# Optimization experiments

Measured on AMD Instinct MI355X. Metric: run time of the kernel, lower is better.

The kernel has to match this reference:

```python
import jax, jax.numpy as jnp
import numpy as np

B, NPTS, T, P, C, D = 2, 32768, 32768, 512, 4, 768


def _sincos_pos_embed(centers, embed_dim):
    # centers: np [P,3]; matches get_3d_sincos_pos_embed
    c = centers - centers.mean(axis=0)
    c = c / np.linalg.norm(c, axis=1).max()
    div = np.exp(np.arange(0, embed_dim, 6) * -(np.log(10000.0) / embed_dim))  # [D/6]
    arg = c[:, None, :] * div[None, :, None]                                   # [P, D/6, 3]
    pe = np.concatenate([np.sin(arg), np.cos(arg)], axis=-1).reshape(centers.shape[0], embed_dim)
    return pe.astype(np.float32)


def setup_inputs() -> dict:
    key = jax.random.key(0)
    ks = jax.random.split(key, 12)
    rng = np.random.default_rng(0)

    # ragged patch sizes (avg 64) summing exactly to T
    sizes = rng.integers(32, 97, size=P).astype(np.int64)
    sizes = np.maximum((sizes * (T / sizes.sum())).astype(np.int64), 1)
    sizes[-1] += T - sizes.sum()
    patch_offset = jnp.asarray(np.concatenate([[0], np.cumsum(sizes)]), dtype=jnp.int32)  # [P+1]

    patch_index = jax.random.randint(ks[0], (T,), 0, NPTS, dtype=jnp.int32)
    latent = jax.random.normal(ks[1], (B, NPTS, C), dtype=jnp.float32)

    s = 0.02
    params = dict(
        w1a=jax.random.normal(ks[2], (C, D), jnp.float32) * s,
        b1a=jnp.zeros((D,), jnp.float32),
        w1b=jax.random.normal(ks[3], (D, D), jnp.float32) * s,
        b1b=jnp.zeros((D,), jnp.float32),
        w2a=jax.random.normal(ks[4], (2 * D, D), jnp.float32) * s,
        b2a=jnp.zeros((D,), jnp.float32),
        g2=jnp.ones((D,), jnp.float32),
        beta2=jnp.zeros((D,), jnp.float32),
        w2b=jax.random.normal(ks[5], (D, D), jnp.float32) * s,
        b2b=jnp.zeros((D,), jnp.float32),
    )

    centers = rng.standard_normal((P, 3))
    pos_embed = jnp.asarray(_sincos_pos_embed(centers, D))[None]  # [1, P, D]

    return dict(latent=latent, patch_index=patch_index, patch_offset=patch_offset,
                pos_embed=pos_embed, **params)


def _ln(x, eps, gamma=None, beta=None):
    mu = x.mean(axis=-1, keepdims=True)
    var = ((x - mu) ** 2).mean(axis=-1, keepdims=True)
    y = (x - mu) * jax.lax.rsqrt(var + eps)
    if gamma is not None:
        y = y * gamma + beta
    return y


def reference(latent, patch_index, patch_offset, pos_embed,
              w1a, b1a, w1b, b1b, w2a, b2a, g2, beta2, w2b, b2b):
    T_ = patch_index.shape[0]
    P_ = patch_offset.shape[0] - 1
    # segment id of each token (repeat_interleave inverse): seg[t] = patch containing t
    seg = jnp.searchsorted(patch_offset[1:], jnp.arange(T_, dtype=patch_offset.dtype), side='right')

    x = latent[:, patch_index, :]                           # [B, T, C] gather
    h = x @ w1a + b1a
    h = jax.nn.gelu(_ln(h, 1e-6), approximate=False)
    h = h @ w1b + b1b                                       # [B, T, D]

    segmax = lambda a: jax.ops.segment_max(a, seg, num_segments=P_)
    y = jax.vmap(segmax)(h)                                 # [B, P, D] ragged max-pool

    h2 = jnp.concatenate([y[:, seg, :], h], axis=-1)        # repeat_interleave + concat
    h2 = h2 @ w2a + b2a
    h2 = jax.nn.gelu(_ln(h2, 1e-5, g2, beta2), approximate=False)
    h2 = h2 @ w2b + b2b                                     # [B, T, D]
    raw_latent = h2

    out = jax.vmap(segmax)(raw_latent) + pos_embed          # [B, P, D]
    return out.astype(raw_latent.dtype), raw_latent
```

## Files before the change

### kernel.cpp

```cpp
#include <hip/hip_runtime.h>
#include <hip/hip_bf16.h>
#include <math.h>

#define B_    2
#define NPTS_ 32768
#define T_    32768
#define P_    512
#define C_    4
#define D_    768
#define M_    (B_ * T_)

typedef __bf16 bf16_t;
typedef __bf16 bf16x8 __attribute__((ext_vector_type(8)));
typedef __bf16 bf16x4 __attribute__((ext_vector_type(4)));
typedef float  f32x4  __attribute__((ext_vector_type(4)));

__device__ inline void gload16(const void* g, void* l) {
  __builtin_amdgcn_global_load_lds(
      (const __attribute__((address_space(1))) void*)g,
      (__attribute__((address_space(3))) void*)l, 16, 0, 0);
}

__device__ inline float gelu_exact(float x) {
  return 0.5f * x * (1.0f + erff(x * 0.70710678118654752f));
}

__device__ inline unsigned fmap(float x) {
  unsigned u = __float_as_uint(x);
  return (u & 0x80000000u) ? ~u : (u | 0x80000000u);
}
__device__ inline float funmap(unsigned u) {
  unsigned v = (u & 0x80000000u) ? (u & 0x7FFFFFFFu) : ~u;
  return __uint_as_float(v);
}

__global__ __launch_bounds__(256) void prep_kernel(
    const int* __restrict__ off, int* __restrict__ seg, uint4* __restrict__ umax,
    const float* __restrict__ w1b, const float* __restrict__ w2a,
    const float* __restrict__ w2b,
    bf16_t* __restrict__ w1bT, bf16_t* __restrict__ w2aTT,
    bf16_t* __restrict__ w2aBT, bf16_t* __restrict__ w2bT) {
  __shared__ float tile[32][33];
  int bid = blockIdx.x, tid = threadIdx.x;
  if (bid < 2304) {
    const float* src; bf16_t* dst;
    int which = bid / 576, r = bid - which * 576;
    if (which == 0)      { src = w1b;             dst = w1bT;  }
    else if (which == 1) { src = w2a;             dst = w2aTT; }
    else if (which == 2) { src = w2a + D_ * D_;   dst = w2aBT; }
    else                 { src = w2b;             dst = w2bT;  }
    int n0 = (r % 24) * 32, k0 = (r / 24) * 32;
    int tx = tid & 31, ty = tid >> 5;
    #pragma unroll
    for (int i = 0; i < 4; ++i)
      tile[ty + 8 * i][tx] = src[(size_t)(k0 + ty + 8 * i) * D_ + n0 + tx];
    __syncthreads();
    #pragma unroll
    for (int i = 0; i < 4; ++i)
      dst[(size_t)(n0 + ty + 8 * i) * D_ + k0 + tx] = (bf16_t)tile[tx][ty + 8 * i];
  } else if (bid < 2432) {
    int t = (bid - 2304) * 256 + tid;
    int lo = 0, hi = P_;
    while (lo < hi) {
      int mid = (lo + hi) >> 1;
      if (off[mid + 1] <= t) lo = mid + 1; else hi = mid;
    }
    seg[t] = lo;
  } else {
    umax[(size_t)(bid - 2432) * 256 + tid] = make_uint4(0, 0, 0, 0);
  }
}

__global__ __launch_bounds__(256) void yconv_kernel(
    const uint4* __restrict__ ymax, bf16_t* __restrict__ y) {
  int t = blockIdx.x * 256 + threadIdx.x;
  uint4 u = ymax[t];
  bf16x4 o;
  o[0] = (bf16_t)funmap(u.x); o[1] = (bf16_t)funmap(u.y);
  o[2] = (bf16_t)funmap(u.z); o[3] = (bf16_t)funmap(u.w);
  *(bf16x4*)(y + (size_t)t * 4) = o;
}

__global__ __launch_bounds__(256) void final2_kernel(
    const uint4* __restrict__ rmax, const float4* __restrict__ pe,
    float4* __restrict__ out) {
  int t = blockIdx.x * 256 + threadIdx.x;
  int row = t / 192, col = t % 192;
  uint4 u = rmax[t];
  float4 p = pe[(row & (P_ - 1)) * 192 + col];
  float4 o;
  o.x = funmap(u.x) + p.x; o.y = funmap(u.y) + p.y;
  o.z = funmap(u.z) + p.z; o.w = funmap(u.w) + p.w;
  out[t] = o;
}

__global__ __launch_bounds__(256) void embed_kernel(
    const float4* __restrict__ latent4, const int* __restrict__ pidx,
    const float* __restrict__ w1a, const float* __restrict__ b1a,
    bf16_t* __restrict__ act1) {
  int wid = threadIdx.x >> 6, lane = threadIdx.x & 63;
  int m = blockIdx.x * 4 + wid;
  int b = m >> 15, t = m & (T_ - 1);
  float4 x = latent4[(size_t)b * NPTS_ + pidx[t]];
  int d8 = lane * 8, d4 = 512 + lane * 4;
  float v[12];
  {
    float4 a0 = *(const float4*)(b1a + d8);
    float4 a1 = *(const float4*)(b1a + d8 + 4);
    float4 a2 = *(const float4*)(b1a + d4);
    v[0]=a0.x; v[1]=a0.y; v[2]=a0.z; v[3]=a0.w;
    v[4]=a1.x; v[5]=a1.y; v[6]=a1.z; v[7]=a1.w;
    v[8]=a2.x; v[9]=a2.y; v[10]=a2.z; v[11]=a2.w;
  }
  float xk[4] = {x.x, x.y, x.z, x.w};
  #pragma unroll
  for (int k = 0; k < 4; ++k) {
    const float* w = w1a + k * D_;
    float4 w0 = *(const float4*)(w + d8);
    float4 w1 = *(const float4*)(w + d8 + 4);
    float4 w2 = *(const float4*)(w + d4);
    float f = xk[k];
    v[0] += f*w0.x; v[1] += f*w0.y; v[2] += f*w0.z; v[3] += f*w0.w;
    v[4] += f*w1.x; v[5] += f*w1.y; v[6] += f*w1.z; v[7] += f*w1.w;
    v[8] += f*w2.x; v[9] += f*w2.y; v[10]+= f*w2.z; v[11]+= f*w2.w;
  }
  float sum = 0.f, sq = 0.f;
  #pragma unroll
  for (int j = 0; j < 12; ++j) { sum += v[j]; sq += v[j]*v[j]; }
  #pragma unroll
  for (int o = 32; o > 0; o >>= 1) { sum += __shfl_xor(sum, o); sq += __shfl_xor(sq, o); }
  float mu = sum * (1.0f / D_);
  float rstd = rsqrtf(sq * (1.0f / D_) - mu * mu + 1e-6f);
  bf16x8 o8; bf16x4 o4;
  #pragma unroll
  for (int j = 0; j < 8; ++j) o8[j] = (bf16_t)gelu_exact((v[j] - mu) * rstd);
  #pragma unroll
  for (int j = 0; j < 4; ++j) o4[j] = (bf16_t)gelu_exact((v[8 + j] - mu) * rstd);
  size_t base = (size_t)m * D_;
  *(bf16x8*)(act1 + base + d8) = o8;
  *(bf16x4*)(act1 + base + d4) = o4;
}

__global__ __launch_bounds__(256) void ln2_kernel(
    const bf16_t* __restrict__ h2pre, const float* __restrict__ z,
    const int* __restrict__ seg, const float* __restrict__ g2,
    const float* __restrict__ beta2, bf16_t* __restrict__ act2) {
  int wid = threadIdx.x >> 6, lane = threadIdx.x & 63;
  int m = blockIdx.x * 4 + wid;
  int b = m >> 15, t = m & (T_ - 1);
  int d8 = lane * 8, d4 = 512 + lane * 4;
  size_t base = (size_t)m * D_;
  const float* zrow = z + (size_t)((b << 9) + seg[t]) * D_;
  bf16x8 i8 = *(const bf16x8*)(h2pre + base + d8);
  bf16x4 i4 = *(const bf16x4*)(h2pre + base + d4);
  float4 z0 = *(const float4*)(zrow + d8);
  float4 z1 = *(const float4*)(zrow + d8 + 4);
  float4 z2 = *(const float4*)(zrow + d4);
  float v[12];
  #pragma unroll
  for (int j = 0; j < 8; ++j) v[j] = (float)i8[j];
  #pragma unroll
  for (int j = 0; j < 4; ++j) v[8 + j] = (float)i4[j];
  v[0]+=z0.x; v[1]+=z0.y; v[2]+=z0.z; v[3]+=z0.w;
  v[4]+=z1.x; v[5]+=z1.y; v[6]+=z1.z; v[7]+=z1.w;
  v[8]+=z2.x; v[9]+=z2.y; v[10]+=z2.z; v[11]+=z2.w;
  float sum = 0.f, sq = 0.f;
  #pragma unroll
  for (int j = 0; j < 12; ++j) { sum += v[j]; sq += v[j]*v[j]; }
  #pragma unroll
  for (int o = 32; o > 0; o >>= 1) { sum += __shfl_xor(sum, o); sq += __shfl_xor(sq, o); }
  float mu = sum * (1.0f / D_);
  float rstd = rsqrtf(sq * (1.0f / D_) - mu * mu + 1e-5f);
  float4 ga = *(const float4*)(g2 + d8);
  float4 gb = *(const float4*)(g2 + d8 + 4);
  float4 gc = *(const float4*)(g2 + d4);
  float4 ba = *(const float4*)(beta2 + d8);
  float4 bb = *(const float4*)(beta2 + d8 + 4);
  float4 bc = *(const float4*)(beta2 + d4);
  float g[12] = {ga.x,ga.y,ga.z,ga.w, gb.x,gb.y,gb.z,gb.w, gc.x,gc.y,gc.z,gc.w};
  float be[12]= {ba.x,ba.y,ba.z,ba.w, bb.x,bb.y,bb.z,bb.w, bc.x,bc.y,bc.z,bc.w};
  bf16x8 o8; bf16x4 o4;
  #pragma unroll
  for (int j = 0; j < 8; ++j) o8[j] = (bf16_t)gelu_exact((v[j] - mu) * rstd * g[j] + be[j]);
  #pragma unroll
  for (int j = 0; j < 4; ++j) o4[j] = (bf16_t)gelu_exact((v[8+j] - mu) * rstd * g[8+j] + be[8+j]);
  *(bf16x8*)(act2 + base + d8) = o8;
  *(bf16x4*)(act2 + base + d4) = o4;
}

#define STAGE_A(P2, KTG)                                                     \
  { _Pragma("unroll")                                                        \
    for (int h = 0; h < 2; ++h) {                                            \
      _Pragma("unroll")                                                      \
      for (int ps = 0; ps < 2; ++ps) {                                       \
        int c = ps * 512 + wid * 64 + lane;                                  \
        int rw = c >> 3;                                                     \
        int cs = (c & 7) ^ (rw & 7);                                         \
        gload16(A + (size_t)(m0 + h * 128 + rw) * 768 + (KTG) + cs * 8,      \
                lds + (P2) * 65536 + h * 16384 + ps * 8192 + wid * 1024);    \
      } } }

#define STAGE_B(P2, KTG)                                                     \
  { _Pragma("unroll")                                                        \
    for (int h = 0; h < 2; ++h) {                                            \
      _Pragma("unroll")                                                      \
      for (int ps = 0; ps < 2; ++ps) {                                       \
        int c = ps * 512 + wid * 64 + lane;                                  \
        int rw = c >> 3;                                                     \
        int cs = (c & 7) ^ (rw & 7);                                         \
        gload16(BT + (size_t)(n0 + h * 128 + rw) * 768 + (KTG) + cs * 8,     \
                lds + (P2) * 65536 + 32768 + h * 16384 + ps * 8192 + wid * 1024); \
      } } }

#define READ_AF0(BASE)                                                       \
  { _Pragma("unroll")                                                        \
    for (int i = 0; i < 4; ++i) {                                            \
      _Pragma("unroll")                                                      \
      for (int s = 0; s < 2; ++s) {                                          \
        int row = i * 16 + lr;                                               \
        int ch = (s * 4 + hi) ^ cx;                                          \
        af0[i][s] = *(const bf16x8*)((BASE) + wm * 16384 + row * 128 + ch * 16); \
      } } }

#define READ_BF0(BASE)                                                       \
  { _Pragma("unroll")                                                        \
    for (int jb = 0; jb < 2; ++jb) {                                         \
      _Pragma("unroll")                                                      \
      for (int s = 0; s < 2; ++s) {                                          \
        int nrow = wn * 64 + jb * 16 + lr;                                   \
        int ch = (s * 4 + hi) ^ cx;                                          \
        bf0[jb][s] = *(const bf16x8*)((BASE) + 32768 + (nrow >> 7) * 16384 + \
                                      (nrow & 127) * 128 + ch * 16);         \
      } } }

template <bool HASBIAS, bool SEGMAX, typename OutT>
__global__ __launch_bounds__(512, 1) void gemm256_kernel(
    const bf16_t* __restrict__ A, const bf16_t* __restrict__ BT,
    const float* __restrict__ bias, OutT* __restrict__ C,
    const int* __restrict__ seg, unsigned* __restrict__ gmax) {
  constexpr int NT = 12;
  __shared__ __align__(16) char lds[131072];
  __shared__ int segm[256];
  int tid = threadIdx.x;
  int wid = tid >> 6, lane = tid & 63;
  int lr = lane & 15, hi = lane >> 4;
  int wm = wid >> 2, wn = wid & 3;

  int gx = gridDim.x;
  int nb = gx * gridDim.y;
  int bid = blockIdx.y * gx + blockIdx.x;
  int w = ((nb & 7) == 0) ? ((bid & 7) * (nb >> 3) + (bid >> 3)) : bid;
  int bx = w % gx, by = w / gx;
  int n0 = bx * 256, m0 = by * 256;

  if (SEGMAX) { if (tid < 256) segm[tid] = seg[(m0 + tid) & (T_ - 1)]; }

  f32x4 acc[8][4] = {};
  bf16x8 af0[4][2], af1[4][2], bf0[2][2], bf1[2][2];
  int cx = lr & 7;

  STAGE_A(0, 0); STAGE_B(0, 0);
  STAGE_A(1, 64); STAGE_B(1, 64);
  asm volatile("s_waitcnt vmcnt(8)" ::: "memory");
  __builtin_amdgcn_s_barrier();
  READ_AF0(lds); READ_BF0(lds);

  for (int j = 0; j < NT; ++j) {
    const char* base  = lds + (j & 1) * 65536;
    const char* baseN = lds + ((j & 1) ^ 1) * 65536;

    #pragma unroll
    for (int i = 0; i < 4; ++i)
      #pragma unroll
      for (int s = 0; s < 2; ++s) {
        int row = 64 + i * 16 + lr;
        int ch = (s * 4 + hi) ^ cx;
        af1[i][s] = *(const bf16x8*)(base + wm * 16384 + row * 128 + ch * 16);
      }
    __builtin_amdgcn_s_setprio(1);
    #pragma unroll
    for (int i = 0; i < 4; ++i)
      #pragma unroll
      for (int jb = 0; jb < 2; ++jb)
        #pragma unroll
        for (int s = 0; s < 2; ++s)
          acc[i][jb] = __builtin_amdgcn_mfma_f32_16x16x32_bf16(bf0[jb][s], af0[i][s], acc[i][jb], 0, 0, 0);
    __builtin_amdgcn_s_setprio(0);
    __builtin_amdgcn_s_barrier();

    #pragma unroll
    for (int jb = 0; jb < 2; ++jb)
      #pragma unroll
      for (int s = 0; s < 2; ++s) {
        int nrow = wn * 64 + 32 + jb * 16 + lr;
        int ch = (s * 4 + hi) ^ cx;
        bf1[jb][s] = *(const bf16x8*)(base + 32768 + (nrow >> 7) * 16384 +
                                      (nrow & 127) * 128 + ch * 16);
      }
    __builtin_amdgcn_s_setprio(1);
    #pragma unroll
    for (int i = 0; i < 4; ++i)
      #pragma unroll
      for (int jb = 0; jb < 2; ++jb)
        #pragma unroll
        for (int s = 0; s < 2; ++s)
          acc[4 + i][jb] = __builtin_amdgcn_mfma_f32_16x16x32_bf16(bf0[jb][s], af1[i][s], acc[4 + i][jb], 0, 0, 0);
    __builtin_amdgcn_s_setprio(0);
    __builtin_amdgcn_s_barrier();

    if (j + 2 < NT) STAGE_A(j & 1, (j + 2) * 64);
    __builtin_amdgcn_s_setprio(1);
    #pragma unroll
    for (int i = 0; i < 4; ++i)
      #pragma unroll
      for (int jb = 0; jb < 2; ++jb)
        #pragma unroll
        for (int s = 0; s < 2; ++s)
          acc[i][2 + jb] = __builtin_amdgcn_mfma_f32_16x16x32_bf16(bf1[jb][s], af0[i][s], acc[i][2 + jb], 0, 0, 0);
    __builtin_amdgcn_s_setprio(0);

    if (j + 1 < NT) {
      if (j + 2 < NT) asm volatile("s_waitcnt vmcnt(4)" ::: "memory");
      else            asm volatile("s_waitcnt vmcnt(0)" ::: "memory");
      __builtin_amdgcn_s_barrier();
      READ_AF0(baseN); READ_BF0(baseN);
      if (j + 2 < NT) STAGE_B(j & 1, (j + 2) * 64);
    }
    __builtin_amdgcn_s_setprio(1);
    #pragma unroll
    for (int i = 0; i < 4; ++i)
      #pragma unroll
      for (int jb = 0; jb < 2; ++jb)
        #pragma unroll
        for (int s = 0; s < 2; ++s)
          acc[4 + i][2 + jb] = __builtin_amdgcn_mfma_f32_16x16x32_bf16(bf1[jb][s], af1[i][s], acc[4 + i][2 + jb], 0, 0, 0);
    __builtin_amdgcn_s_setprio(0);
    __builtin_amdgcn_s_barrier();
  }

  unsigned* smax = reinterpret_cast<unsigned*>(lds);
  int sb = 0, zb = 0;
  if (SEGMAX) {
    sb = segm[0];
    zb = (m0 >> 15) << 9;
    for (int q = tid; q < 16 * 256; q += 512) smax[q] = 0u;
    __syncthreads();
  }

  f32x4 bvv[4];
  #pragma unroll
  for (int jb = 0; jb < 4; ++jb) {
    if (HASBIAS) {
      const float* bp = bias + n0 + wn * 64 + jb * 16 + hi * 4;
      bvv[jb][0] = bp[0]; bvv[jb][1] = bp[1]; bvv[jb][2] = bp[2]; bvv[jb][3] = bp[3];
    } else {
      bvv[jb][0] = bvv[jb][1] = bvv[jb][2] = bvv[jb][3] = 0.f;
    }
  }

  #pragma unroll
  for (int i = 0; i < 8; ++i) {
    size_t ro = (size_t)(m0 + wm * 128 + i * 16 + lr) * 768 + (n0 + wn * 64 + hi * 4);
    #pragma unroll
    for (int jb = 0; jb < 4; ++jb) {
      f32x4 v = acc[i][jb] + bvv[jb];
      if constexpr (sizeof(OutT) == 4) {
        *reinterpret_cast<f32x4*>(C + ro + jb * 16) = v;
      } else {
        bf16x4 o;
        #pragma unroll
        for (int r = 0; r < 4; ++r) o[r] = (bf16_t)v[r];
        *reinterpret_cast<bf16x4*>(C + ro + jb * 16) = o;
      }
    }
  }

  if (SEGMAX) {
    int lrow = wm * 128 + lr;
    #pragma unroll
    for (int jb = 0; jb < 4; ++jb) {
      int nl = wn * 64 + jb * 16 + hi * 4;
      f32x4 run = acc[0][jb] + bvv[jb];
      int ps = segm[lrow];
      #pragma unroll
      for (int i = 1; i < 8; ++i) {
        int cs2 = segm[lrow + i * 16];
        f32x4 v = acc[i][jb] + bvv[jb];
        if (cs2 != ps) {
          #pragma unroll
          for (int r = 0; r < 4; ++r)
            atomicMax(&smax[(ps - sb) * 256 + nl + r], fmap(run[r]));
          run = v; ps = cs2;
        } else {
          #pragma unroll
          for (int r = 0; r < 4; ++r) run[r] = fmaxf(run[r], v[r]);
        }
      }
      #pragma unroll
      for (int r = 0; r < 4; ++r)
        atomicMax(&smax[(ps - sb) * 256 + nl + r], fmap(run[r]));
    }
    __syncthreads();
    int nseg = segm[255] - sb + 1;
    int mlo = m0 & (T_ - 1);
    bool strad_lo = (mlo != 0) && (seg[(mlo - 1)] == sb);
    bool strad_hi = (mlo + 256 < T_) && (seg[(mlo + 256)] == segm[255]);
    for (int q = tid; q < nseg * 256; q += 512) {
      int sl = q >> 8, nl2 = q & 255;
      unsigned val = smax[q];
      unsigned* dst = &gmax[(size_t)(zb + sb + sl) * 768 + n0 + nl2];
      bool bdry = (sl == 0 && strad_lo) || (sl == nseg - 1 && strad_hi);
      if (bdry) atomicMax(dst, val);
      else      *dst = val;
    }
  }
}

extern "C" void kernel_launch(void* const* d_in, const int* in_sizes, int n_in,
                              void* d_out, int out_size, void* d_ws, size_t ws_size,
                              hipStream_t stream) {
  const float* latent       = (const float*)d_in[0];
  const int*   patch_index  = (const int*)d_in[1];
  const int*   patch_offset = (const int*)d_in[2];
  const float* pos_embed    = (const float*)d_in[3];
  const float* w1a  = (const float*)d_in[4];
  const float* b1a  = (const float*)d_in[5];
  const float* w1b  = (const float*)d_in[6];
  const float* b1b  = (const float*)d_in[7];
  const float* w2a  = (const float*)d_in[8];
  const float* b2a  = (const float*)d_in[9];
  const float* g2   = (const float*)d_in[10];
  const float* beta2= (const float*)d_in[11];
  const float* w2b  = (const float*)d_in[12];
  const float* b2b  = (const float*)d_in[13];

  float* out_f   = (float*)d_out;
  float* raw_out = out_f + (size_t)B_ * P_ * D_;

  char* ws = (char*)d_ws;
  size_t off = 0;
  auto take = [&](size_t bytes) {
    off = (off + 255) & ~(size_t)255;
    char* p = ws + off;
    off += bytes;
    return p;
  };
  int*      seg   = (int*)     take((size_t)T_ * 4);
  bf16_t*   w1bT  = (bf16_t*)  take((size_t)D_ * D_ * 2);
  bf16_t*   w2aTT = (bf16_t*)  take((size_t)D_ * D_ * 2);
  bf16_t*   w2aBT = (bf16_t*)  take((size_t)D_ * D_ * 2);
  bf16_t*   w2bT  = (bf16_t*)  take((size_t)D_ * D_ * 2);
  bf16_t*   ybuf  = (bf16_t*)  take((size_t)B_ * P_ * D_ * 2);
  float*    zbuf  = (float*)   take((size_t)B_ * P_ * D_ * 4);
  unsigned* umax  = (unsigned*)take((size_t)2 * B_ * P_ * D_ * 4);
  unsigned* ymax  = umax;
  unsigned* rmax  = umax + (size_t)B_ * P_ * D_;
  bf16_t*   bufY  = (bf16_t*)  take((size_t)M_ * D_ * 2);
  size_t needX = (size_t)M_ * D_ * 2;
  size_t offX  = (off + 255) & ~(size_t)255;
  bf16_t* bufX;
  if (offX + needX <= ws_size) {
    bufX = (bf16_t*)take(needX);
  } else {
    bufX = (bf16_t*)raw_out;
  }

  prep_kernel<<<3968, 256, 0, stream>>>(patch_offset, seg, (uint4*)umax,
                                        w1b, w2a, w2b, w1bT, w2aTT, w2aBT, w2bT);

  embed_kernel<<<M_ / 4, 256, 0, stream>>>((const float4*)latent, patch_index, w1a, b1a, bufX);

  gemm256_kernel<true, true, bf16_t><<<dim3(3, M_/256), 512, 0, stream>>>(
      bufX, w1bT, b1b, bufY, seg, ymax);

  yconv_kernel<<<(B_ * P_ * D_) / (4 * 256), 256, 0, stream>>>((const uint4*)ymax, ybuf);

  gemm256_kernel<true, false, float><<<dim3(3, (B_*P_)/256), 512, 0, stream>>>(
      ybuf, w2aTT, b2a, zbuf, nullptr, nullptr);

  gemm256_kernel<false, false, bf16_t><<<dim3(3, M_/256), 512, 0, stream>>>(
      bufY, w2aBT, nullptr, bufX, nullptr, nullptr);

  ln2_kernel<<<M_ / 4, 256, 0, stream>>>(bufX, zbuf, seg, g2, beta2, bufY);

  gemm256_kernel<true, true, float><<<dim3(3, M_/256), 512, 0, stream>>>(
      bufY, w2bT, b2b, raw_out, seg, rmax);

  final2_kernel<<<(B_ * P_ * D_) / (4 * 256), 256, 0, stream>>>(
      (const uint4*)rmax, (const float4*)pos_embed, (float4*)out_f);
}
```

Before: 440.3 us.

## Replace fused GEMM-epilogue segment max with standalone per-patch reduction kernels

Removes the segment-max logic from the GEMM epilogue: the shared-memory atomicMax, the order-preserving uint mapping, the global atomics and the umax zeroing. Two standalone kernels take its place, one block per (batch, patch), each re-reading the stored activations to compute the ragged max. The final kernel also adds the positional embedding. This drops the yconv and final2 passes and the epilogue atomics, but re-reads the full bf16 h tensor and the fp32 raw_latent tensor from global memory, so memory traffic rises substantially.

After: 477.8 us. 1.09x slower.

```diff
diff --git a/kernel.cpp b/kernel.cpp
--- a/kernel.cpp
+++ b/kernel.cpp
@@ -25,17 +25,8 @@
   return 0.5f * x * (1.0f + erff(x * 0.70710678118654752f));
 }
 
-__device__ inline unsigned fmap(float x) {
-  unsigned u = __float_as_uint(x);
-  return (u & 0x80000000u) ? ~u : (u | 0x80000000u);
-}
-__device__ inline float funmap(unsigned u) {
-  unsigned v = (u & 0x80000000u) ? (u & 0x7FFFFFFFu) : ~u;
-  return __uint_as_float(v);
-}
-
 __global__ __launch_bounds__(256) void prep_kernel(
-    const int* __restrict__ off, int* __restrict__ seg, uint4* __restrict__ umax,
+    const int* __restrict__ off, int* __restrict__ seg,
     const float* __restrict__ w1b, const float* __restrict__ w2a,
     const float* __restrict__ w2b,
     bf16_t* __restrict__ w1bT, bf16_t* __restrict__ w2aTT,
@@ -58,7 +49,7 @@
     #pragma unroll
     for (int i = 0; i < 4; ++i)
       dst[(size_t)(n0 + ty + 8 * i) * D_ + k0 + tx] = (bf16_t)tile[tx][ty + 8 * i];
-  } else if (bid < 2432) {
+  } else {
     int t = (bid - 2304) * 256 + tid;
     int lo = 0, hi = P_;
     while (lo < hi) {
@@ -66,32 +57,7 @@
       if (off[mid + 1] <= t) lo = mid + 1; else hi = mid;
     }
     seg[t] = lo;
-  } else {
-    umax[(size_t)(bid - 2432) * 256 + tid] = make_uint4(0, 0, 0, 0);
-  }
-}
-
-__global__ __launch_bounds__(256) void yconv_kernel(
-    const uint4* __restrict__ ymax, bf16_t* __restrict__ y) {
-  int t = blockIdx.x * 256 + threadIdx.x;
-  uint4 u = ymax[t];
-  bf16x4 o;
-  o[0] = (bf16_t)funmap(u.x); o[1] = (bf16_t)funmap(u.y);
-  o[2] = (bf16_t)funmap(u.z); o[3] = (bf16_t)funmap(u.w);
-  *(bf16x4*)(y + (size_t)t * 4) = o;
-}
-
-__global__ __launch_bounds__(256) void final2_kernel(
-    const uint4* __restrict__ rmax, const float4* __restrict__ pe,
-    float4* __restrict__ out) {
-  int t = blockIdx.x * 256 + threadIdx.x;
-  int row = t / 192, col = t % 192;
-  uint4 u = rmax[t];
-  float4 p = pe[(row & (P_ - 1)) * 192 + col];
-  float4 o;
-  o.x = funmap(u.x) + p.x; o.y = funmap(u.y) + p.y;
-  o.z = funmap(u.z) + p.z; o.w = funmap(u.w) + p.w;
-  out[t] = o;
+  }
 }
 
 __global__ __launch_bounds__(256) void embed_kernel(
@@ -188,6 +154,101 @@
   *(bf16x4*)(act2 + base + d4) = o4;
 }
 
+__global__ __launch_bounds__(256) void segmax_kernel(
+    const bf16_t* __restrict__ h, const int* __restrict__ off,
+    bf16_t* __restrict__ y) {
+  int bp = blockIdx.x;
+  int b = bp >> 9, p = bp & (P_ - 1);
+  int t0 = off[p], t1 = off[p + 1];
+  int wid = threadIdx.x >> 6, lane = threadIdx.x & 63;
+  int d8 = lane * 8, d4 = 512 + lane * 4;
+  const bf16_t* hb = h + (size_t)b * T_ * D_;
+  float mx[12];
+  #pragma unroll
+  for (int j = 0; j < 12; ++j) mx[j] = -INFINITY;
+  for (int t = t0 + wid; t < t1; t += 4) {
+    const bf16_t* row = hb + (size_t)t * D_;
+    bf16x8 a = *(const bf16x8*)(row + d8);
+    bf16x4 c = *(const bf16x4*)(row + d4);
+    #pragma unroll
+    for (int j = 0; j < 8; ++j) mx[j] = fmaxf(mx[j], (float)a[j]);
+    #pragma unroll
+    for (int j = 0; j < 4; ++j) mx[8 + j] = fmaxf(mx[8 + j], (float)c[j]);
+  }
+  __shared__ float pm[4][D_];
+  #pragma unroll
+  for (int j = 0; j < 8; ++j) pm[wid][d8 + j] = mx[j];
+  #pragma unroll
+  for (int j = 0; j < 4; ++j) pm[wid][d4 + j] = mx[8 + j];
+  __syncthreads();
+  if (wid == 0) {
+    bf16x8 o8; bf16x4 o4;
+    #pragma unroll
+    for (int j = 0; j < 8; ++j) {
+      int d = d8 + j;
+      o8[j] = (bf16_t)fmaxf(fmaxf(pm[0][d], pm[1][d]), fmaxf(pm[2][d], pm[3][d]));
+    }
+    #pragma unroll
+    for (int j = 0; j < 4; ++j) {
+      int d = d4 + j;
+      o4[j] = (bf16_t)fmaxf(fmaxf(pm[0][d], pm[1][d]), fmaxf(pm[2][d], pm[3][d]));
+    }
+    *(bf16x8*)(y + (size_t)bp * D_ + d8) = o8;
+    *(bf16x4*)(y + (size_t)bp * D_ + d4) = o4;
+  }
+}
+
+__global__ __launch_bounds__(256) void final_kernel(
+    const float* __restrict__ raw, const int* __restrict__ off,
+    const float* __restrict__ pe, float* __restrict__ out) {
+  int bp = blockIdx.x;
+  int b = bp >> 9, p = bp & (P_ - 1);
+  int t0 = off[p], t1 = off[p + 1];
+  int wid = threadIdx.x >> 6, lane = threadIdx.x & 63;
+  int d8 = lane * 8, d4 = 512 + lane * 4;
+  const float* rb = raw + (size_t)b * T_ * D_;
+  float mx[12];
+  #pragma unroll
+  for (int j = 0; j < 12; ++j) mx[j] = -INFINITY;
+  for (int t = t0 + wid; t < t1; t += 4) {
+    const float* row = rb + (size_t)t * D_;
+    float4 r0 = *(const float4*)(row + d8);
+    float4 r1 = *(const float4*)(row + d8 + 4);
+    float4 r2 = *(const float4*)(row + d4);
+    mx[0]=fmaxf(mx[0],r0.x); mx[1]=fmaxf(mx[1],r0.y); mx[2]=fmaxf(mx[2],r0.z); mx[3]=fmaxf(mx[3],r0.w);
+    mx[4]=fmaxf(mx[4],r1.x); mx[5]=fmaxf(mx[5],r1.y); mx[6]=fmaxf(mx[6],r1.z); mx[7]=fmaxf(mx[7],r1.w);
+    mx[8]=fmaxf(mx[8],r2.x); mx[9]=fmaxf(mx[9],r2.y); mx[10]=fmaxf(mx[10],r2.z); mx[11]=fmaxf(mx[11],r2.w);
+  }
+  __shared__ float pm[4][D_];
+  #pragma unroll
+  for (int j = 0; j < 8; ++j) pm[wid][d8 + j] = mx[j];
+  #pragma unroll
+  for (int j = 0; j < 4; ++j) pm[wid][d4 + j] = mx[8 + j];
+  __syncthreads();
+  if (wid == 0) {
+    const float* per = pe + (size_t)p * D_;
+    float* orow = out + (size_t)bp * D_;
+    float r[12];
+    #pragma unroll
+    for (int j = 0; j < 8; ++j) {
+      int d = d8 + j;
+      r[j] = fmaxf(fmaxf(pm[0][d], pm[1][d]), fmaxf(pm[2][d], pm[3][d])) + per[d];
+    }
+    #pragma unroll
+    for (int j = 0; j < 4; ++j) {
+      int d = d4 + j;
+      r[8 + j] = fmaxf(fmaxf(pm[0][d], pm[1][d]), fmaxf(pm[2][d], pm[3][d])) + per[d];
+    }
+    float4 o0, o1, o2;
+    o0.x=r[0]; o0.y=r[1]; o0.z=r[2]; o0.w=r[3];
+    o1.x=r[4]; o1.y=r[5]; o1.z=r[6]; o1.w=r[7];
+    o2.x=r[8]; o2.y=r[9]; o2.z=r[10]; o2.w=r[11];
+    *(float4*)(orow + d8) = o0;
+    *(float4*)(orow + d8 + 4) = o1;
+    *(float4*)(orow + d4) = o2;
+  }
+}
+
 #define STAGE_A(P2, KTG)                                                     \
   { _Pragma("unroll")                                                        \
     for (int h = 0; h < 2; ++h) {                                            \
@@ -233,14 +294,12 @@
                                       (nrow & 127) * 128 + ch * 16);         \
       } } }
 
-template <bool HASBIAS, bool SEGMAX, typename OutT>
+template <bool HASBIAS, typename OutT>
 __global__ __launch_bounds__(512, 1) void gemm256_kernel(
     const bf16_t* __restrict__ A, const bf16_t* __restrict__ BT,
-    const float* __restrict__ bias, OutT* __restrict__ C,
-    const int* __restrict__ seg, unsigned* __restrict__ gmax) {
+    const float* __restrict__ bias, OutT* __restrict__ C) {
   constexpr int NT = 12;
   __shared__ __align__(16) char lds[131072];
-  __shared__ int segm[256];
   int tid = threadIdx.x;
   int wid = tid >> 6, lane = tid & 63;
   int lr = lane & 15, hi = lane >> 4;
@@ -252,8 +311,6 @@
   int w = ((nb & 7) == 0) ? ((bid & 7) * (nb >> 3) + (bid >> 3)) : bid;
   int bx = w % gx, by = w / gx;
   int n0 = bx * 256, m0 = by * 256;
-
-  if (SEGMAX) { if (tid < 256) segm[tid] = seg[(m0 + tid) & (T_ - 1)]; }
 
   f32x4 acc[8][4] = {};
   bf16x8 af0[4][2], af1[4][2], bf0[2][2], bf1[2][2];
@@ -338,15 +395,6 @@
     __builtin_amdgcn_s_barrier();
   }
 
-  unsigned* smax = reinterpret_cast<unsigned*>(lds);
-  int sb = 0, zb = 0;
-  if (SEGMAX) {
-    sb = segm[0];
-    zb = (m0 >> 15) << 9;
-    for (int q = tid; q < 16 * 256; q += 512) smax[q] = 0u;
-    __syncthreads();
-  }
-
   f32x4 bvv[4];
   #pragma unroll
   for (int jb = 0; jb < 4; ++jb) {
@@ -357,7 +405,6 @@
       bvv[jb][0] = bvv[jb][1] = bvv[jb][2] = bvv[jb][3] = 0.f;
     }
   }
-
   #pragma unroll
   for (int i = 0; i < 8; ++i) {
     size_t ro = (size_t)(m0 + wm * 128 + i * 16 + lr) * 768 + (n0 + wn * 64 + hi * 4);
@@ -372,46 +419,6 @@
         for (int r = 0; r < 4; ++r) o[r] = (bf16_t)v[r];
         *reinterpret_cast<bf16x4*>(C + ro + jb * 16) = o;
       }
-    }
-  }
-
-  if (SEGMAX) {
-    int lrow = wm * 128 + lr;
-    #pragma unroll
-    for (int jb = 0; jb < 4; ++jb) {
-      int nl = wn * 64 + jb * 16 + hi * 4;
-      f32x4 run = acc[0][jb] + bvv[jb];
-      int ps = segm[lrow];
-      #pragma unroll
-      for (int i = 1; i < 8; ++i) {
-        int cs2 = segm[lrow + i * 16];
-        f32x4 v = acc[i][jb] + bvv[jb];
-        if (cs2 != ps) {
-          #pragma unroll
-          for (int r = 0; r < 4; ++r)
-            atomicMax(&smax[(ps - sb) * 256 + nl + r], fmap(run[r]));
-          run = v; ps = cs2;
-        } else {
-          #pragma unroll
-          for (int r = 0; r < 4; ++r) run[r] = fmaxf(run[r], v[r]);
-        }
-      }
-      #pragma unroll
-      for (int r = 0; r < 4; ++r)
-        atomicMax(&smax[(ps - sb) * 256 + nl + r], fmap(run[r]));
-    }
-    __syncthreads();
-    int nseg = segm[255] - sb + 1;
-    int mlo = m0 & (T_ - 1);
-    bool strad_lo = (mlo != 0) && (seg[(mlo - 1)] == sb);
-    bool strad_hi = (mlo + 256 < T_) && (seg[(mlo + 256)] == segm[255]);
-    for (int q = tid; q < nseg * 256; q += 512) {
-      int sl = q >> 8, nl2 = q & 255;
-      unsigned val = smax[q];
-      unsigned* dst = &gmax[(size_t)(zb + sb + sl) * 768 + n0 + nl2];
-      bool bdry = (sl == 0 && strad_lo) || (sl == nseg - 1 && strad_hi);
-      if (bdry) atomicMax(dst, val);
-      else      *dst = val;
     }
   }
 }
@@ -452,9 +459,6 @@
   bf16_t*   w2bT  = (bf16_t*)  take((size_t)D_ * D_ * 2);
   bf16_t*   ybuf  = (bf16_t*)  take((size_t)B_ * P_ * D_ * 2);
   float*    zbuf  = (float*)   take((size_t)B_ * P_ * D_ * 4);
-  unsigned* umax  = (unsigned*)take((size_t)2 * B_ * P_ * D_ * 4);
-  unsigned* ymax  = umax;
-  unsigned* rmax  = umax + (size_t)B_ * P_ * D_;
   bf16_t*   bufY  = (bf16_t*)  take((size_t)M_ * D_ * 2);
   size_t needX = (size_t)M_ * D_ * 2;
   size_t offX  = (off + 255) & ~(size_t)255;
@@ -465,27 +469,26 @@
     bufX = (bf16_t*)raw_out;
   }
 
-  prep_kernel<<<3968, 256, 0, stream>>>(patch_offset, seg, (uint4*)umax,
+  prep_kernel<<<2432, 256, 0, stream>>>(patch_offset, seg,
                                         w1b, w2a, w2b, w1bT, w2aTT, w2aBT, w2bT);
 
   embed_kernel<<<M_ / 4, 256, 0, stream>>>((const float4*)latent, patch_index, w1a, b1a, bufX);
 
-  gemm256_kernel<true, true, bf16_t><<<dim3(3, M_/256), 512, 0, stream>>>(
-      bufX, w1bT, b1b, bufY, seg, ymax);
-
-  yconv_kernel<<<(B_ * P_ * D_) / (4 * 256), 256, 0, stream>>>((const uint4*)ymax, ybuf);
-
-  gemm256_kernel<true, false, float><<<dim3(3, (B_*P_)/256), 512, 0, stream>>>(
-      ybuf, w2aTT, b2a, zbuf, nullptr, nullptr);
-
-  gemm256_kernel<false, false, bf16_t><<<dim3(3, M_/256), 512, 0, stream>>>(
-      bufY, w2aBT, nullptr, bufX, nullptr, nullptr);
+  gemm256_kernel<true, bf16_t><<<dim3(3, M_/256), 512, 0, stream>>>(
+      bufX, w1bT, b1b, bufY);
+
+  segmax_kernel<<<B_ * P_, 256, 0, stream>>>(bufY, patch_offset, ybuf);
+
+  gemm256_kernel<true, float><<<dim3(3, (B_*P_)/256), 512, 0, stream>>>(
+      ybuf, w2aTT, b2a, zbuf);
+
+  gemm256_kernel<false, bf16_t><<<dim3(3, M_/256), 512, 0, stream>>>(
+      bufY, w2aBT, nullptr, bufX);
 
   ln2_kernel<<<M_ / 4, 256, 0, stream>>>(bufX, zbuf, seg, g2, beta2, bufY);
 
-  gemm256_kernel<true, true, float><<<dim3(3, M_/256), 512, 0, stream>>>(
-      bufY, w2bT, b2b, raw_out, seg, rmax);
-
-  final2_kernel<<<(B_ * P_ * D_) / (4 * 256), 256, 0, stream>>>(
-      (const uint4*)rmax, (const float4*)pos_embed, (float4*)out_f);
-}
+  gemm256_kernel<true, float><<<dim3(3, M_/256), 512, 0, stream>>>(
+      bufY, w2bT, b2b, raw_out);
+
+  final_kernel<<<B_ * P_, 256, 0, stream>>>(raw_out, patch_offset, pos_embed, out_f);
+}
```

## Merge embed into prep kernel, fuse yconv with GEMM, shuffle-reduce segmax epilogue

Applied to the files above, without the earlier changes.

Folds the embed stage into the prep kernel, with each wave handling four rows and keeping w1a and b1a in registers. Fuses the ymax-to-bf16 conversion into the large h@w2a-bottom GEMM launch as extra blocks, and reorders the small z GEMM after it. The segment-max epilogue now does a cross-lane shuffle max over 16-row groups that lie in one segment, which cuts LDS atomics. The aim is fewer launches and less atomic contention, at the cost of more branching and register pressure in the fused kernels.

New measurement: 499.1 us. +13.3%, slower.

```diff
diff --git a/kernel.cpp b/kernel.cpp
--- a/kernel.cpp
+++ b/kernel.cpp
@@ -34,17 +34,72 @@
   return __uint_as_float(v);
 }
 
-__global__ __launch_bounds__(256) void prep_kernel(
+__global__ __launch_bounds__(256) void bigprep_kernel(
+    const float4* __restrict__ latent4, const int* __restrict__ pidx,
+    const float* __restrict__ w1a, const float* __restrict__ b1a,
+    bf16_t* __restrict__ act1,
     const int* __restrict__ off, int* __restrict__ seg, uint4* __restrict__ umax,
     const float* __restrict__ w1b, const float* __restrict__ w2a,
     const float* __restrict__ w2b,
     bf16_t* __restrict__ w1bT, bf16_t* __restrict__ w2aTT,
     bf16_t* __restrict__ w2aBT, bf16_t* __restrict__ w2bT) {
-  __shared__ float tile[32][33];
   int bid = blockIdx.x, tid = threadIdx.x;
-  if (bid < 2304) {
+  if (bid < 4096) {
+    int wid = tid >> 6, lane = tid & 63;
+    int mb = bid * 16 + wid * 4;
+    int d8 = lane * 8, d4 = 512 + lane * 4;
+    float bb[12], wreg[4][12];
+    {
+      float4 a0 = *(const float4*)(b1a + d8);
+      float4 a1 = *(const float4*)(b1a + d8 + 4);
+      float4 a2 = *(const float4*)(b1a + d4);
+      bb[0]=a0.x; bb[1]=a0.y; bb[2]=a0.z; bb[3]=a0.w;
+      bb[4]=a1.x; bb[5]=a1.y; bb[6]=a1.z; bb[7]=a1.w;
+      bb[8]=a2.x; bb[9]=a2.y; bb[10]=a2.z; bb[11]=a2.w;
+    }
+    #pragma unroll
+    for (int k = 0; k < 4; ++k) {
+      const float* w = w1a + k * D_;
+      float4 w0 = *(const float4*)(w + d8);
+      float4 w1 = *(const float4*)(w + d8 + 4);
+      float4 w2 = *(const float4*)(w + d4);
+      wreg[k][0]=w0.x; wreg[k][1]=w0.y; wreg[k][2]=w0.z; wreg[k][3]=w0.w;
+      wreg[k][4]=w1.x; wreg[k][5]=w1.y; wreg[k][6]=w1.z; wreg[k][7]=w1.w;
+      wreg[k][8]=w2.x; wreg[k][9]=w2.y; wreg[k][10]=w2.z; wreg[k][11]=w2.w;
+    }
+    for (int rr = 0; rr < 4; ++rr) {
+      int m = mb + rr;
+      int b = m >> 15, t = m & (T_ - 1);
+      float4 x = latent4[(size_t)b * NPTS_ + pidx[t]];
+      float xk[4] = {x.x, x.y, x.z, x.w};
+      float v[12];
+      #pragma unroll
+      for (int j = 0; j < 12; ++j) {
+        v[j] = bb[j];
+        #pragma unroll
+        for (int k = 0; k < 4; ++k) v[j] += xk[k] * wreg[k][j];
+      }
+      float sum = 0.f, sq = 0.f;
+      #pragma unroll
+      for (int j = 0; j < 12; ++j) { sum += v[j]; sq += v[j]*v[j]; }
+      #pragma unroll
+      for (int o = 32; o > 0; o >>= 1) { sum += __shfl_xor(sum, o); sq += __shfl_xor(sq, o); }
+      float mu = sum * (1.0f / D_);
+      float rstd = rsqrtf(sq * (1.0f / D_) - mu * mu + 1e-6f);
+      bf16x8 o8; bf16x4 o4;
+      #pragma unroll
+      for (int j = 0; j < 8; ++j) o8[j] = (bf16_t)gelu_exact((v[j] - mu) * rstd);
+      #pragma unroll
+      for (int j = 0; j < 4; ++j) o4[j] = (bf16_t)gelu_exact((v[8 + j] - mu) * rstd);
+      size_t base = (size_t)m * D_;
+      *(bf16x8*)(act1 + base + d8) = o8;
+      *(bf16x4*)(act1 + base + d4) = o4;
+    }
+  } else if (bid < 6400) {
+    __shared__ float tile[32][33];
+    int r = bid - 4096;
     const float* src; bf16_t* dst;
-    int which = bid / 576, r = bid - which * 576;
+    int which = r / 576; r -= which * 576;
     if (which == 0)      { src = w1b;             dst = w1bT;  }
     else if (which == 1) { src = w2a;             dst = w2aTT; }
     else if (which == 2) { src = w2a + D_ * D_;   dst = w2aBT; }
@@ -58,8 +113,8 @@
     #pragma unroll
     for (int i = 0; i < 4; ++i)
       dst[(size_t)(n0 + ty + 8 * i) * D_ + k0 + tx] = (bf16_t)tile[tx][ty + 8 * i];
-  } else if (bid < 2432) {
-    int t = (bid - 2304) * 256 + tid;
+  } else if (bid < 6528) {
+    int t = (bid - 6400) * 256 + tid;
     int lo = 0, hi = P_;
     while (lo < hi) {
       int mid = (lo + hi) >> 1;
@@ -67,78 +122,8 @@
     }
     seg[t] = lo;
   } else {
-    umax[(size_t)(bid - 2432) * 256 + tid] = make_uint4(0, 0, 0, 0);
-  }
-}
-
-__global__ __launch_bounds__(256) void yconv_kernel(
-    const uint4* __restrict__ ymax, bf16_t* __restrict__ y) {
-  int t = blockIdx.x * 256 + threadIdx.x;
-  uint4 u = ymax[t];
-  bf16x4 o;
-  o[0] = (bf16_t)funmap(u.x); o[1] = (bf16_t)funmap(u.y);
-  o[2] = (bf16_t)funmap(u.z); o[3] = (bf16_t)funmap(u.w);
-  *(bf16x4*)(y + (size_t)t * 4) = o;
-}
-
-__global__ __launch_bounds__(256) void final2_kernel(
-    const uint4* __restrict__ rmax, const float4* __restrict__ pe,
-    float4* __restrict__ out) {
-  int t = blockIdx.x * 256 + threadIdx.x;
-  int row = t / 192, col = t % 192;
-  uint4 u = rmax[t];
-  float4 p = pe[(row & (P_ - 1)) * 192 + col];
-  float4 o;
-  o.x = funmap(u.x) + p.x; o.y = funmap(u.y) + p.y;
-  o.z = funmap(u.z) + p.z; o.w = funmap(u.w) + p.w;
-  out[t] = o;
-}
-
-__global__ __launch_bounds__(256) void embed_kernel(
-    const float4* __restrict__ latent4, const int* __restrict__ pidx,
-    const float* __restrict__ w1a, const float* __restrict__ b1a,
-    bf16_t* __restrict__ act1) {
-  int wid = threadIdx.x >> 6, lane = threadIdx.x & 63;
-  int m = blockIdx.x * 4 + wid;
-  int b = m >> 15, t = m & (T_ - 1);
-  float4 x = latent4[(size_t)b * NPTS_ + pidx[t]];
-  int d8 = lane * 8, d4 = 512 + lane * 4;
-  float v[12];
-  {
-    float4 a0 = *(const float4*)(b1a + d8);
-    float4 a1 = *(const float4*)(b1a + d8 + 4);
-    float4 a2 = *(const float4*)(b1a + d4);
-    v[0]=a0.x; v[1]=a0.y; v[2]=a0.z; v[3]=a0.w;
-    v[4]=a1.x; v[5]=a1.y; v[6]=a1.z; v[7]=a1.w;
-    v[8]=a2.x; v[9]=a2.y; v[10]=a2.z; v[11]=a2.w;
-  }
-  float xk[4] = {x.x, x.y, x.z, x.w};
-  #pragma unroll
-  for (int k = 0; k < 4; ++k) {
-    const float* w = w1a + k * D_;
-    float4 w0 = *(const float4*)(w + d8);
-    float4 w1 = *(const float4*)(w + d8 + 4);
-    float4 w2 = *(const float4*)(w + d4);
-    float f = xk[k];
-    v[0] += f*w0.x; v[1] += f*w0.y; v[2] += f*w0.z; v[3] += f*w0.w;
-    v[4] += f*w1.x; v[5] += f*w1.y; v[6] += f*w1.z; v[7] += f*w1.w;
-    v[8] += f*w2.x; v[9] += f*w2.y; v[10]+= f*w2.z; v[11]+= f*w2.w;
-  }
-  float sum = 0.f, sq = 0.f;
-  #pragma unroll
-  for (int j = 0; j < 12; ++j) { sum += v[j]; sq += v[j]*v[j]; }
-  #pragma unroll
-  for (int o = 32; o > 0; o >>= 1) { sum += __shfl_xor(sum, o); sq += __shfl_xor(sq, o); }
-  float mu = sum * (1.0f / D_);
-  float rstd = rsqrtf(sq * (1.0f / D_) - mu * mu + 1e-6f);
-  bf16x8 o8; bf16x4 o4;
-  #pragma unroll
-  for (int j = 0; j < 8; ++j) o8[j] = (bf16_t)gelu_exact((v[j] - mu) * rstd);
-  #pragma unroll
-  for (int j = 0; j < 4; ++j) o4[j] = (bf16_t)gelu_exact((v[8 + j] - mu) * rstd);
-  size_t base = (size_t)m * D_;
-  *(bf16x8*)(act1 + base + d8) = o8;
-  *(bf16x4*)(act1 + base + d4) = o4;
+    umax[(size_t)(bid - 6528) * 256 + tid] = make_uint4(0, 0, 0, 0);
+  }
 }
 
 __global__ __launch_bounds__(256) void ln2_kernel(
@@ -175,10 +160,10 @@
   float4 gb = *(const float4*)(g2 + d8 + 4);
   float4 gc = *(const float4*)(g2 + d4);
   float4 ba = *(const float4*)(beta2 + d8);
-  float4 bb = *(const float4*)(beta2 + d8 + 4);
+  float4 bbv = *(const float4*)(beta2 + d8 + 4);
   float4 bc = *(const float4*)(beta2 + d4);
   float g[12] = {ga.x,ga.y,ga.z,ga.w, gb.x,gb.y,gb.z,gb.w, gc.x,gc.y,gc.z,gc.w};
-  float be[12]= {ba.x,ba.y,ba.z,ba.w, bb.x,bb.y,bb.z,bb.w, bc.x,bc.y,bc.z,bc.w};
+  float be[12]= {ba.x,ba.y,ba.z,ba.w, bbv.x,bbv.y,bbv.z,bbv.w, bc.x,bc.y,bc.z,bc.w};
   bf16x8 o8; bf16x4 o4;
   #pragma unroll
   for (int j = 0; j < 8; ++j) o8[j] = (bf16_t)gelu_exact((v[j] - mu) * rstd * g[j] + be[j]);
@@ -186,6 +171,19 @@
   for (int j = 0; j < 4; ++j) o4[j] = (bf16_t)gelu_exact((v[8+j] - mu) * rstd * g[8+j] + be[8+j]);
   *(bf16x8*)(act2 + base + d8) = o8;
   *(bf16x4*)(act2 + base + d4) = o4;
+}
+
+__global__ __launch_bounds__(256) void final2_kernel(
+    const uint4* __restrict__ rmax, const float4* __restrict__ pe,
+    float4* __restrict__ out) {
+  int t = blockIdx.x * 256 + threadIdx.x;
+  int row = t / 192, col = t % 192;
+  uint4 u = rmax[t];
+  float4 p = pe[(row & (P_ - 1)) * 192 + col];
+  float4 o;
+  o.x = funmap(u.x) + p.x; o.y = funmap(u.y) + p.y;
+  o.z = funmap(u.z) + p.z; o.w = funmap(u.w) + p.w;
+  out[t] = o;
 }
 
 #define STAGE_A(P2, KTG)                                                     \
@@ -234,7 +232,8 @@
       } } }
 
 template <bool HASBIAS, bool SEGMAX, typename OutT>
-__global__ __launch_bounds__(512, 1) void gemm256_kernel(
+__device__ __forceinline__ void gemm256_body(
+    int bid, int nbx, int nby,
     const bf16_t* __restrict__ A, const bf16_t* __restrict__ BT,
     const float* __restrict__ bias, OutT* __restrict__ C,
     const int* __restrict__ seg, unsigned* __restrict__ gmax) {
@@ -246,11 +245,9 @@
   int lr = lane & 15, hi = lane >> 4;
   int wm = wid >> 2, wn = wid & 3;
 
-  int gx = gridDim.x;
-  int nb = gx * gridDim.y;
-  int bid = blockIdx.y * gx + blockIdx.x;
+  int nb = nbx * nby;
   int w = ((nb & 7) == 0) ? ((bid & 7) * (nb >> 3) + (bid >> 3)) : bid;
-  int bx = w % gx, by = w / gx;
+  int bx = w % nbx, by = w / nbx;
   int n0 = bx * 256, m0 = by * 256;
 
   if (SEGMAX) { if (tid < 256) segm[tid] = seg[(m0 + tid) & (T_ - 1)]; }
@@ -338,15 +335,6 @@
     __builtin_amdgcn_s_barrier();
   }
 
-  unsigned* smax = reinterpret_cast<unsigned*>(lds);
-  int sb = 0, zb = 0;
-  if (SEGMAX) {
-    sb = segm[0];
-    zb = (m0 >> 15) << 9;
-    for (int q = tid; q < 16 * 256; q += 512) smax[q] = 0u;
-    __syncthreads();
-  }
-
   f32x4 bvv[4];
   #pragma unroll
   for (int jb = 0; jb < 4; ++jb) {
@@ -357,7 +345,6 @@
       bvv[jb][0] = bvv[jb][1] = bvv[jb][2] = bvv[jb][3] = 0.f;
     }
   }
-
   #pragma unroll
   for (int i = 0; i < 8; ++i) {
     size_t ro = (size_t)(m0 + wm * 128 + i * 16 + lr) * 768 + (n0 + wn * 64 + hi * 4);
@@ -376,35 +363,61 @@
   }
 
   if (SEGMAX) {
-    int lrow = wm * 128 + lr;
+    unsigned* smax = reinterpret_cast<unsigned*>(lds);
+    __builtin_amdgcn_s_barrier();
+    int sb = segm[0];
+    int zb = (m0 >> 15) << 9;
+    for (int q = tid; q < 16 * 256; q += 512) smax[q] = 0u;
+    __syncthreads();
+
+    int lrow0 = wm * 128;
     #pragma unroll
     for (int jb = 0; jb < 4; ++jb) {
       int nl = wn * 64 + jb * 16 + hi * 4;
-      f32x4 run = acc[0][jb] + bvv[jb];
-      int ps = segm[lrow];
-      #pragma unroll
-      for (int i = 1; i < 8; ++i) {
-        int cs2 = segm[lrow + i * 16];
-        f32x4 v = acc[i][jb] + bvv[jb];
-        if (cs2 != ps) {
+      auto flush = [&](f32x4& V, int S) {
+        #pragma unroll
+        for (int o = 1; o < 16; o <<= 1) {
+          V[0] = fmaxf(V[0], __shfl_xor(V[0], o));
+          V[1] = fmaxf(V[1], __shfl_xor(V[1], o));
+          V[2] = fmaxf(V[2], __shfl_xor(V[2], o));
+          V[3] = fmaxf(V[3], __shfl_xor(V[3], o));
+        }
+        if (lr == 0) {
           #pragma unroll
           for (int r = 0; r < 4; ++r)
-            atomicMax(&smax[(ps - sb) * 256 + nl + r], fmap(run[r]));
-          run = v; ps = cs2;
+            atomicMax(&smax[(S - sb) * 256 + nl + r], fmap(V[r]));
+        }
+      };
+      bool have = false; f32x4 runv; int runs = 0;
+      #pragma unroll
+      for (int i = 0; i < 8; ++i) {
+        int g0 = lrow0 + i * 16;
+        int sA = segm[g0], sB = segm[g0 + 15];
+        f32x4 v = acc[i][jb] + bvv[jb];
+        if (sA == sB) {
+          if (have && runs == sA) {
+            #pragma unroll
+            for (int r = 0; r < 4; ++r) runv[r] = fmaxf(runv[r], v[r]);
+          } else {
+            if (have) flush(runv, runs);
+            runv = v; runs = sA; have = true;
+          }
         } else {
+          if (have) { flush(runv, runs); have = false; }
+          int sM = segm[g0 + lr];
           #pragma unroll
-          for (int r = 0; r < 4; ++r) run[r] = fmaxf(run[r], v[r]);
+          for (int r = 0; r < 4; ++r)
+            atomicMax(&smax[(sM - sb) * 256 + nl + r], fmap(v[r]));
         }
       }
-      #pragma unroll
-      for (int r = 0; r < 4; ++r)
-        atomicMax(&smax[(ps - sb) * 256 + nl + r], fmap(run[r]));
+      if (have) flush(runv, runs);
     }
     __syncthreads();
+
     int nseg = segm[255] - sb + 1;
     int mlo = m0 & (T_ - 1);
-    bool strad_lo = (mlo != 0) && (seg[(mlo - 1)] == sb);
-    bool strad_hi = (mlo + 256 < T_) && (seg[(mlo + 256)] == segm[255]);
+    bool strad_lo = (mlo != 0) && (seg[mlo - 1] == sb);
+    bool strad_hi = (mlo + 256 < T_) && (seg[mlo + 256] == segm[255]);
     for (int q = tid; q < nseg * 256; q += 512) {
       int sl = q >> 8, nl2 = q & 255;
       unsigned val = smax[q];
@@ -413,6 +426,34 @@
       if (bdry) atomicMax(dst, val);
       else      *dst = val;
     }
+  }
+}
+
+template <bool HASBIAS, bool SEGMAX, typename OutT>
+__global__ __launch_bounds__(512, 1) void gemm256_kernel(
+    const bf16_t* __restrict__ A, const bf16_t* __restrict__ BT,
+    const float* __restrict__ bias, OutT* __restrict__ C,
+    const int* __restrict__ seg, unsigned* __restrict__ gmax) {
+  gemm256_body<HASBIAS, SEGMAX, OutT>(
+      blockIdx.y * gridDim.x + blockIdx.x, gridDim.x, gridDim.y,
+      A, BT, bias, C, seg, gmax);
+}
+
+__global__ __launch_bounds__(512, 1) void g2_yconv_kernel(
+    const bf16_t* __restrict__ A, const bf16_t* __restrict__ BT,
+    bf16_t* __restrict__ C,
+    const uint4* __restrict__ ymax, bf16_t* __restrict__ y) {
+  int bid = blockIdx.x;
+  if (bid < 768) {
+    gemm256_body<false, false, bf16_t>(bid, 3, 256, A, BT, nullptr, C,
+                                       nullptr, nullptr);
+  } else {
+    int t = (bid - 768) * 512 + threadIdx.x;
+    uint4 u = ymax[t];
+    bf16x4 o;
+    o[0] = (bf16_t)funmap(u.x); o[1] = (bf16_t)funmap(u.y);
+    o[2] = (bf16_t)funmap(u.z); o[3] = (bf16_t)funmap(u.w);
+    *(bf16x4*)(y + (size_t)t * 4) = o;
   }
 }
 
@@ -465,27 +506,25 @@
     bufX = (bf16_t*)raw_out;
   }
 
-  prep_kernel<<<3968, 256, 0, stream>>>(patch_offset, seg, (uint4*)umax,
-                                        w1b, w2a, w2b, w1bT, w2aTT, w2aBT, w2bT);
-
-  embed_kernel<<<M_ / 4, 256, 0, stream>>>((const float4*)latent, patch_index, w1a, b1a, bufX);
+  bigprep_kernel<<<8064, 256, 0, stream>>>(
+      (const float4*)latent, patch_index, w1a, b1a, bufX,
+      patch_offset, seg, (uint4*)umax,
+      w1b, w2a, w2b, w1bT, w2aTT, w2aBT, w2bT);
 
   gemm256_kernel<true, true, bf16_t><<<dim3(3, M_/256), 512, 0, stream>>>(
       bufX, w1bT, b1b, bufY, seg, ymax);
 
-  yconv_kernel<<<(B_ * P_ * D_) / (4 * 256), 256, 0, stream>>>((const uint4*)ymax, ybuf);
-
-  gemm256_kernel<true, false, float><<<dim3(3, (B_*P_)/256), 512, 0, stream>>>(
+  g2_yconv_kernel<<<1152, 512, 0, stream>>>(
+      bufY, w2aBT, bufX, (const uint4*)ymax, ybuf);
+
+  gemm256_kernel<true, false, float><<<dim3(3, 4), 512, 0, stream>>>(
       ybuf, w2aTT, b2a, zbuf, nullptr, nullptr);
-
-  gemm256_kernel<false, false, bf16_t><<<dim3(3, M_/256), 512, 0, stream>>>(
-      bufY, w2aBT, nullptr, bufX, nullptr, nullptr);
 
   ln2_kernel<<<M_ / 4, 256, 0, stream>>>(bufX, zbuf, seg, g2, beta2, bufY);
 
   gemm256_kernel<true, true, float><<<dim3(3, M_/256), 512, 0, stream>>>(
       bufY, w2bT, b2b, raw_out, seg, rmax);
 
-  final2_kernel<<<(B_ * P_ * D_) / (4 * 256), 256, 0, stream>>>(
+  final2_kernel<<<768, 256, 0, stream>>>(
       (const uint4*)rmax, (const float4*)pos_embed, (float4*)out_f);
 }
```
